# Kernel optimization log

Measured on AMD Instinct MI355X. Metric: run time of the kernel, lower is better.

Reference implementation:

```python
import jax, jax.numpy as jnp
import numpy as np

B, S, D, H = 4, 2048, 1024, 16
HD = D // H  # head dim = 64


def setup_inputs() -> dict:
    key = jax.random.key(0)
    ks = jax.random.split(key, 10)
    std = 1.0 / np.sqrt(D)
    return {
        "Q": jax.random.normal(ks[0], (B, S, D), jnp.float32),
        "Q_lev": jax.random.normal(ks[1], (B, S, D), jnp.float32),
        "K": jax.random.normal(ks[2], (B, S, D), jnp.float32),
        "K_lev": jax.random.normal(ks[3], (B, S, D), jnp.float32),
        "V": jax.random.normal(ks[4], (B, S, D), jnp.float32),
        "V_lev": jax.random.normal(ks[5], (B, S, D), jnp.float32),
        "Wq": jax.random.normal(ks[6], (D, D), jnp.float32) * std,
        "bq": jnp.zeros((D,), jnp.float32),
        "Wk": jax.random.normal(ks[7], (D, D), jnp.float32) * std,
        "bk": jnp.zeros((D,), jnp.float32),
        "Wv": jax.random.normal(ks[8], (D, D), jnp.float32) * std,
        "bv": jnp.zeros((D,), jnp.float32),
        "Wo": jax.random.normal(ks[9], (D, D), jnp.float32) * std,
        "bo": jnp.zeros((D,), jnp.float32),
    }


def _heads(x):
    # [B,S,D] -> [B,H,S,HD]
    return x.reshape(B, S, H, HD).transpose(0, 2, 1, 3)


def reference(Q, Q_lev, K, K_lev, V, V_lev, Wq, bq, Wk, bk, Wv, bv, Wo, bo):
    q = _heads(Q @ Wq + bq + Q_lev)
    k = _heads(K @ Wk + bk + K_lev)
    v = _heads(V @ Wv + bv + V_lev)
    scores = jnp.einsum("bhqd,bhkd->bhqk", q, k) / np.sqrt(HD).astype(np.float32)
    probs = jax.nn.softmax(scores, axis=-1)  # attn_dropout rate 0 -> identity
    ctx = jnp.einsum("bhqk,bhkd->bhqd", probs, v)
    ctx = ctx.transpose(0, 2, 1, 3).reshape(B, S, D)
    return ctx @ Wo + bo  # proj_dropout rate 0 -> identity
```

## Files before the change

### kernel.cpp

```cpp
#include <hip/hip_runtime.h>
#include <hip/hip_bf16.h>

#define Bq 4
#define Sq 2048
#define Dq 1024
#define Hq 16
#define HDq 64
#define MR (Bq*Sq)

typedef __attribute__((ext_vector_type(8))) short bf16x8;
typedef __attribute__((ext_vector_type(4))) float f32x4;
typedef __attribute__((ext_vector_type(16))) float f32x16;

__device__ __forceinline__ unsigned short f2bf(float f){
  unsigned int x = __builtin_bit_cast(unsigned int, f);
  x += 0x7fffu + ((x >> 16) & 1u);
  return (unsigned short)(x >> 16);
}

#define MFMA(a,b,c)   __builtin_amdgcn_mfma_f32_16x16x32_bf16((a),(b),(c),0,0,0)
#define MFMA32(a,b,c) __builtin_amdgcn_mfma_f32_32x32x16_bf16((a),(b),(c),0,0,0)

#define SC_Q 0.18033688f

__global__ __launch_bounds__(256) void transpose_w(
    const float* __restrict__ W0, const float* __restrict__ W1,
    const float* __restrict__ W2, const float* __restrict__ W3,
    unsigned short* __restrict__ T0, unsigned short* __restrict__ T1,
    unsigned short* __restrict__ T2, unsigned short* __restrict__ T3)
{
  __shared__ float tile[32][33];
  const int z = blockIdx.z;
  const float* W = z==0?W0 : z==1?W1 : z==2?W2 : W3;
  unsigned short* T = z==0?T0 : z==1?T1 : z==2?T2 : T3;
  const int k0 = blockIdx.x*32, n0 = blockIdx.y*32;
  const int tx = threadIdx.x & 31, ty = threadIdx.x >> 5;
  #pragma unroll
  for (int i=0;i<4;i++) tile[ty+i*8][tx] = W[(size_t)(k0+ty+i*8)*Dq + n0+tx];
  __syncthreads();
  #pragma unroll
  for (int i=0;i<4;i++) T[(size_t)(n0+ty+i*8)*Dq + k0+tx] = f2bf(tile[tx][ty+i*8]);
}

__global__ __launch_bounds__(256) void transpose_v(
    const unsigned short* __restrict__ Vb, unsigned short* __restrict__ Vo)
{
  __shared__ unsigned short t2[64][72];
  const int bh = blockIdx.y;
  const int b = bh >> 4, h = bh & 15;
  const int s0 = blockIdx.x * 64;
  const int tid = threadIdx.x;
  const int r = tid >> 3, c8 = tid & 7;
  #pragma unroll
  for (int i=0;i<2;i++){
    int s = r + i*32;
    union { int4 v; unsigned short u[8]; } uu;
    uu.v = *(const int4*)(Vb + ((size_t)b*Sq + s0 + s)*Dq + h*HDq + c8*8);
    #pragma unroll
    for (int jj=0;jj<8;jj++){
      int j = (jj + c8) & 7;
      t2[c8*8 + j][s] = uu.u[j];
    }
  }
  __syncthreads();
  #pragma unroll
  for (int i=0;i<2;i++){
    int d = r + i*32;
    *(int4*)(Vo + ((size_t)bh*HDq + d)*Sq + s0 + c8*8) = *(const int4*)&t2[d][c8*8];
  }
}

template<bool AF32>
__device__ __forceinline__ void gemm_loop(const void* __restrict__ Ap,
    const unsigned short* __restrict__ Bt,
    int bm, int bn, unsigned short* Al, unsigned short* Bl, f32x4 acc[4][4])
{
  const int tid = threadIdx.x;
  const int lane = tid & 63, wid = tid >> 6;
  const int lr = lane & 15, lg = lane >> 4;
  const int wm = wid >> 1, wn = wid & 1;

  for (int k0 = 0; k0 < Dq; k0 += 64) {
    __syncthreads();
    if (AF32) {
      const float* A = (const float*)Ap;
      #pragma unroll
      for (int i=0;i<8;i++){
        int slot = tid + 256*i;
        int row = slot >> 4, sl = slot & 15;
        const float4 d = *(const float4*)(A + (size_t)(bm*128+row)*Dq + k0 + sl*4);
        union { unsigned short u[4]; unsigned long long v; } pk;
        pk.u[0]=f2bf(d.x); pk.u[1]=f2bf(d.y); pk.u[2]=f2bf(d.z); pk.u[3]=f2bf(d.w);
        *(unsigned long long*)(Al + row*72 + sl*4) = pk.v;
      }
    } else {
      const unsigned short* A = (const unsigned short*)Ap;
      #pragma unroll
      for (int i=0;i<4;i++){
        int slot = tid + 256*i;
        int row = slot >> 3, sl = slot & 7;
        *(int4*)(Al + row*72 + sl*8) = *(const int4*)(A + (size_t)(bm*128+row)*Dq + k0 + sl*8);
      }
    }
    #pragma unroll
    for (int i=0;i<4;i++){
      int slot = tid + 256*i;
      int row = slot >> 3, sl = slot & 7;
      *(int4*)(Bl + row*72 + sl*8) = *(const int4*)(Bt + (size_t)(bn*128+row)*Dq + k0 + sl*8);
    }
    __syncthreads();
    #pragma unroll
    for (int kc=0;kc<2;kc++){
      bf16x8 af[4], bfr[4];
      #pragma unroll
      for (int mt=0;mt<4;mt++) af[mt]  = *(const bf16x8*)(Al + (wm*64+mt*16+lr)*72 + kc*32 + lg*8);
      #pragma unroll
      for (int nt=0;nt<4;nt++) bfr[nt] = *(const bf16x8*)(Bl + (wn*64+nt*16+lr)*72 + kc*32 + lg*8);
      #pragma unroll
      for (int mt=0;mt<4;mt++)
        #pragma unroll
        for (int nt=0;nt<4;nt++)
          acc[mt][nt] = MFMA(af[mt], bfr[nt], acc[mt][nt]);
    }
  }
}

__global__ __launch_bounds__(256) void proj_gemm(
    const float* __restrict__ Aq, const float* __restrict__ Ak, const float* __restrict__ Av,
    const float* __restrict__ Lq, const float* __restrict__ Lk, const float* __restrict__ Lv,
    const unsigned short* __restrict__ Tq, const unsigned short* __restrict__ Tk, const unsigned short* __restrict__ Tv,
    const float* __restrict__ bqp, const float* __restrict__ bkp, const float* __restrict__ bvp,
    unsigned short* __restrict__ Oq, unsigned short* __restrict__ Ok, unsigned short* __restrict__ Ov)
{
  __shared__ unsigned short Al[128*72];
  __shared__ unsigned short Bl[128*72];
  const int z = blockIdx.z;
  const float* A   = z==0?Aq : z==1?Ak : Av;
  const float* Lev = z==0?Lq : z==1?Lk : Lv;
  const unsigned short* Bt = z==0?Tq : z==1?Tk : Tv;
  const float* bias = z==0?bqp : z==1?bkp : bvp;
  unsigned short* Out = z==0?Oq : z==1?Ok : Ov;
  const float scl = (z==0) ? SC_Q : 1.0f;

  f32x4 acc[4][4];
  #pragma unroll
  for (int mt=0;mt<4;mt++)
    #pragma unroll
    for (int nt=0;nt<4;nt++) acc[mt][nt] = (f32x4){0.f,0.f,0.f,0.f};

  gemm_loop<true>(A, Bt, blockIdx.x, blockIdx.y, Al, Bl, acc);

  const int tid = threadIdx.x, lane = tid&63, wid = tid>>6;
  const int lr = lane&15, lg = lane>>4, wm = wid>>1, wn = wid&1;
  const int colb = blockIdx.y*128 + wn*64;
  float bcol[4];
  #pragma unroll
  for (int nt=0;nt<4;nt++) bcol[nt] = bias[colb + nt*16 + lr];
  #pragma unroll
  for (int mt=0;mt<4;mt++){
    int g = blockIdx.x*128 + wm*64 + mt*16 + lg*4;
    #pragma unroll
    for (int r=0;r<4;r++){
      size_t ro = (size_t)(g+r)*Dq;
      #pragma unroll
      for (int nt=0;nt<4;nt++){
        int col = colb + nt*16 + lr;
        float v = (acc[mt][nt][r] + bcol[nt] + Lev[ro + col]) * scl;
        Out[ro + col] = f2bf(v);
      }
    }
  }
}

__device__ __forceinline__ float comb_max(float x){ return fmaxf(x, __shfl_xor(x, 32, 64)); }
__device__ __forceinline__ float comb_sum(float x){ return x + __shfl_xor(x, 32, 64); }

__device__ __forceinline__ void pack_p(const f32x16& t, int hi, bf16x8& c0, bf16x8& c1){
  unsigned w[8];
  #pragma unroll
  for (int j=0;j<8;j++)
    w[j] = (unsigned)f2bf(t[2*j]) | ((unsigned)f2bf(t[2*j+1]) << 16);
  unsigned x[8];
  #pragma unroll
  for (int j=0;j<8;j++) x[j] = (unsigned)__shfl_xor((int)w[j], 32, 64);
  union { unsigned u[4]; bf16x8 v; } p0, p1;
  p0.u[0] = hi ? x[2] : w[0];
  p0.u[1] = hi ? x[3] : w[1];
  p0.u[2] = hi ? w[2] : x[0];
  p0.u[3] = hi ? w[3] : x[1];
  p1.u[0] = hi ? x[6] : w[4];
  p1.u[1] = hi ? x[7] : w[5];
  p1.u[2] = hi ? w[6] : x[4];
  p1.u[3] = hi ? w[7] : x[5];
  c0 = p0.v; c1 = p1.v;
}

__global__ __launch_bounds__(512, 4) void attn_k(
    const unsigned short* qb, const unsigned short* __restrict__ kb,
    const unsigned short* __restrict__ vt, unsigned short* cb)
{
  __shared__ unsigned short Kl[2][64*64];
  __shared__ unsigned short Vl[2][64*64];
  __shared__ float Rl[8][32];

  const int bid = blockIdx.x;
  const int swz = (bid & 7)*64 + (bid >> 3);
  const int qt = swz & 7, bh = swz >> 3;
  const int b = bh >> 4, h = bh & 15;
  const size_t base = (size_t)b*Sq*Dq + (size_t)h*HDq;

  const int tid = threadIdx.x, lane = tid & 63, wid = tid >> 6;
  const int ln31 = lane & 31, hi = lane >> 5;
  const int q0 = qt*256 + wid*32;

  bf16x8 qf[4];
  {
    const unsigned short* qp = qb + base + (size_t)(q0 + ln31)*Dq + hi*8;
    #pragma unroll
    for (int dk=0;dk<4;dk++) qf[dk] = *(const bf16x8*)(qp + dk*16);
  }

  const int kRow = tid >> 3, kCh = tid & 7;
  const unsigned short* kSrc = kb + base + (size_t)kRow*Dq + kCh*8;
  const unsigned short* vSrc = vt + ((size_t)bh*HDq + kRow)*Sq + kCh*8;
  const int wOff = kRow*64 + ((kCh ^ (kRow & 7))*8);

  int4 kreg = *(const int4*)kSrc;
  int4 vreg = *(const int4*)vSrc;
  *(int4*)&Kl[0][wOff] = kreg;
  *(int4*)&Vl[0][wOff] = vreg;

  f32x16 o0 = (f32x16)(0.0f), o1 = (f32x16)(0.0f);
  float m = -1e30f, l = 0.f;

  for (int kt = 0; kt < Sq/64; ++kt){
    __syncthreads();
    const int p = kt & 1;
    if (kt+1 < Sq/64){
      kreg = *(const int4*)(kSrc + (size_t)(kt+1)*64*Dq);
      vreg = *(const int4*)(vSrc + (kt+1)*64);
    }

    f32x16 t0 = (f32x16)(0.0f), t1 = (f32x16)(0.0f);
    __builtin_amdgcn_s_setprio(1);
    #pragma unroll
    for (int dk=0;dk<4;dk++){
      const int c = hi + dk*2;
      bf16x8 kf0 = *(const bf16x8*)&Kl[p][(ln31)*64    + ((c ^ (ln31 & 7))*8)];
      bf16x8 kf1 = *(const bf16x8*)&Kl[p][(32+ln31)*64 + ((c ^ (ln31 & 7))*8)];
      t0 = MFMA32(kf0, qf[dk], t0);
      t1 = MFMA32(kf1, qf[dk], t1);
    }
    __builtin_amdgcn_s_setprio(0);

    float tmax = t0[0];
    #pragma unroll
    for (int r=1;r<16;r++) tmax = fmaxf(tmax, t0[r]);
    #pragma unroll
    for (int r=0;r<16;r++) tmax = fmaxf(tmax, t1[r]);
    tmax = comb_max(tmax);
    if (__any(tmax > m + 8.0f)){
      float mn = fmaxf(m, tmax);
      float al = __builtin_amdgcn_exp2f(m - mn);
      m = mn;
      l *= al;
      if (hi == 0) Rl[wid][ln31] = al;
      asm volatile("" ::: "memory");
      f32x4 av[4];
      #pragma unroll
      for (int g=0; g<4; g++) av[g] = *(const f32x4*)&Rl[wid][g*8 + hi*4];
      #pragma unroll
      for (int r=0;r<16;r++){ o0[r] *= av[r>>2][r&3]; o1[r] *= av[r>>2][r&3]; }
    }
    float tsum = 0.f;
    #pragma unroll
    for (int r=0;r<16;r++){
      float a0 = __builtin_amdgcn_exp2f(t0[r] - m); t0[r] = a0; tsum += a0;
      float a1 = __builtin_amdgcn_exp2f(t1[r] - m); t1[r] = a1; tsum += a1;
    }
    l += comb_sum(tsum);

    bf16x8 pa0, pa1, pa2, pa3;
    pack_p(t0, hi, pa0, pa1);
    pack_p(t1, hi, pa2, pa3);
    __builtin_amdgcn_s_setprio(1);
    #pragma unroll
    for (int c=0;c<4;c++){
      bf16x8 pa = c==0?pa0 : c==1?pa1 : c==2?pa2 : pa3;
      const int vc = 2*c + hi;
      bf16x8 vf0 = *(const bf16x8*)&Vl[p][(ln31)*64    + ((vc ^ (ln31 & 7))*8)];
      bf16x8 vf1 = *(const bf16x8*)&Vl[p][(32+ln31)*64 + ((vc ^ (ln31 & 7))*8)];
      o0 = MFMA32(pa, vf0, o0);
      o1 = MFMA32(pa, vf1, o1);
    }
    __builtin_amdgcn_s_setprio(0);

    if (kt+1 < Sq/64){
      const int pn = p ^ 1;
      *(int4*)&Kl[pn][wOff] = kreg;
      *(int4*)&Vl[pn][wOff] = vreg;
    }
  }

  float linv = __builtin_amdgcn_rcpf(l);
  if (hi == 0) Rl[wid][ln31] = linv;
  asm volatile("" ::: "memory");
  f32x4 lv[4];
  #pragma unroll
  for (int g=0; g<4; g++) lv[g] = *(const f32x4*)&Rl[wid][g*8 + hi*4];
  #pragma unroll
  for (int r=0;r<16;r++){
    int q = (r&3) + 8*(r>>2) + 4*hi;
    size_t ro = base + (size_t)(q0 + q)*Dq;
    cb[ro + ln31]      = f2bf(o0[r] * lv[r>>2][r&3]);
    cb[ro + 32 + ln31] = f2bf(o1[r] * lv[r>>2][r&3]);
  }
}

__global__ __launch_bounds__(256) void out_gemm(
    const unsigned short* __restrict__ Ctx, const unsigned short* __restrict__ To,
    const float* __restrict__ bop, float* __restrict__ Out)
{
  __shared__ unsigned short Al[128*72];
  __shared__ unsigned short Bl[128*72];
  f32x4 acc[4][4];
  #pragma unroll
  for (int mt=0;mt<4;mt++)
    #pragma unroll
    for (int nt=0;nt<4;nt++) acc[mt][nt] = (f32x4){0.f,0.f,0.f,0.f};

  gemm_loop<false>(Ctx, To, blockIdx.x, blockIdx.y, Al, Bl, acc);

  const int tid = threadIdx.x, lane = tid&63, wid = tid>>6;
  const int lr = lane&15, lg = lane>>4, wm = wid>>1, wn = wid&1;
  const int colb = blockIdx.y*128 + wn*64;
  float bcol[4];
  #pragma unroll
  for (int nt=0;nt<4;nt++) bcol[nt] = bop[colb + nt*16 + lr];
  #pragma unroll
  for (int mt=0;mt<4;mt++){
    int g = blockIdx.x*128 + wm*64 + mt*16 + lg*4;
    #pragma unroll
    for (int r=0;r<4;r++){
      size_t ro = (size_t)(g+r)*Dq;
      #pragma unroll
      for (int nt=0;nt<4;nt++){
        int col = colb + nt*16 + lr;
        Out[ro + col] = acc[mt][nt][r] + bcol[nt];
      }
    }
  }
}

extern "C" void kernel_launch(void* const* d_in, const int* in_sizes, int n_in,
                              void* d_out, int out_size, void* d_ws, size_t ws_size,
                              hipStream_t stream) {
  const float* Q    = (const float*)d_in[0];
  const float* Qlev = (const float*)d_in[1];
  const float* K    = (const float*)d_in[2];
  const float* Klev = (const float*)d_in[3];
  const float* V    = (const float*)d_in[4];
  const float* Vlev = (const float*)d_in[5];
  const float* Wq   = (const float*)d_in[6];
  const float* bq   = (const float*)d_in[7];
  const float* Wk   = (const float*)d_in[8];
  const float* bk   = (const float*)d_in[9];
  const float* Wv   = (const float*)d_in[10];
  const float* bv   = (const float*)d_in[11];
  const float* Wo   = (const float*)d_in[12];
  const float* bo   = (const float*)d_in[13];

  unsigned short* qbuf = (unsigned short*)d_ws;
  unsigned short* kbuf = qbuf + (size_t)MR*Dq;
  unsigned short* vbuf = kbuf + (size_t)MR*Dq;
  unsigned short* vtb  = vbuf + (size_t)MR*Dq;
  unsigned short* Tq   = vtb  + (size_t)MR*Dq;
  unsigned short* Tk   = Tq + (size_t)Dq*Dq;
  unsigned short* Tv   = Tk + (size_t)Dq*Dq;
  unsigned short* To   = Tv + (size_t)Dq*Dq;

  transpose_w<<<dim3(Dq/32, Dq/32, 4), 256, 0, stream>>>(Wq,Wk,Wv,Wo, Tq,Tk,Tv,To);
  proj_gemm<<<dim3(MR/128, Dq/128, 3), 256, 0, stream>>>(
      Q,K,V, Qlev,Klev,Vlev, Tq,Tk,Tv, bq,bk,bv, qbuf,kbuf,vbuf);
  transpose_v<<<dim3(Sq/64, Bq*Hq), 256, 0, stream>>>(vbuf, vtb);
  attn_k<<<dim3(512), 512, 0, stream>>>(qbuf, kbuf, vtb, qbuf);
  out_gemm<<<dim3(MR/128, Dq/128), 256, 0, stream>>>(qbuf, To, bo, (float*)d_out);
}
```

Measured before the change: 273.0 us.

## Pre-convert activations to bf16 and stage GEMM tiles with direct global-to-LDS loads

```diff
diff --git a/kernel.cpp b/kernel.cpp
--- a/kernel.cpp
+++ b/kernel.cpp
@@ -23,6 +23,28 @@
 
 #define SC_Q 0.18033688f
 
+__device__ __forceinline__ void gload16(const unsigned short* g, unsigned short* l){
+  __builtin_amdgcn_global_load_lds(
+      (const __attribute__((address_space(1))) void*)g,
+      (__attribute__((address_space(3))) void*)l, 16, 0, 0);
+}
+
+__global__ __launch_bounds__(256) void cvt_bf16x3(
+    const float* __restrict__ X0, const float* __restrict__ X1, const float* __restrict__ X2,
+    unsigned short* __restrict__ O0, unsigned short* __restrict__ O1, unsigned short* __restrict__ O2)
+{
+  const int z = blockIdx.y;
+  const float* X = z==0?X0 : z==1?X1 : X2;
+  unsigned short* O = z==0?O0 : z==1?O1 : O2;
+  const size_t i = ((size_t)blockIdx.x*256 + threadIdx.x)*8;
+  const float4 a = *(const float4*)(X+i);
+  const float4 b = *(const float4*)(X+i+4);
+  union { unsigned short u[8]; int4 v; } pk;
+  pk.u[0]=f2bf(a.x); pk.u[1]=f2bf(a.y); pk.u[2]=f2bf(a.z); pk.u[3]=f2bf(a.w);
+  pk.u[4]=f2bf(b.x); pk.u[5]=f2bf(b.y); pk.u[6]=f2bf(b.z); pk.u[7]=f2bf(b.w);
+  *(int4*)(O+i) = pk.v;
+}
+
 __global__ __launch_bounds__(256) void transpose_w(
     const float* __restrict__ W0, const float* __restrict__ W1,
     const float* __restrict__ W2, const float* __restrict__ W3,
@@ -70,8 +92,7 @@
   }
 }
 
-template<bool AF32>
-__device__ __forceinline__ void gemm_loop(const void* __restrict__ Ap,
+__device__ __forceinline__ void gemm_loop(const unsigned short* __restrict__ A,
     const unsigned short* __restrict__ Bt,
     int bm, int bn, unsigned short* Al, unsigned short* Bl, f32x4 acc[4][4])
 {
@@ -80,42 +101,28 @@
   const int lr = lane & 15, lg = lane >> 4;
   const int wm = wid >> 1, wn = wid & 1;
 
+  const int srow = wid*32 + (lane >> 3), sch = (lane & 7)*8;
+  const unsigned short* As = A  + (size_t)(bm*128 + srow)*Dq + sch;
+  const unsigned short* Bs = Bt + (size_t)(bn*128 + srow)*Dq + sch;
+  unsigned short* Ald = Al + wid*2048;
+  unsigned short* Bld = Bl + wid*2048;
+
   for (int k0 = 0; k0 < Dq; k0 += 64) {
     __syncthreads();
-    if (AF32) {
-      const float* A = (const float*)Ap;
-      #pragma unroll
-      for (int i=0;i<8;i++){
-        int slot = tid + 256*i;
-        int row = slot >> 4, sl = slot & 15;
-        const float4 d = *(const float4*)(A + (size_t)(bm*128+row)*Dq + k0 + sl*4);
-        union { unsigned short u[4]; unsigned long long v; } pk;
-        pk.u[0]=f2bf(d.x); pk.u[1]=f2bf(d.y); pk.u[2]=f2bf(d.z); pk.u[3]=f2bf(d.w);
-        *(unsigned long long*)(Al + row*72 + sl*4) = pk.v;
-      }
-    } else {
-      const unsigned short* A = (const unsigned short*)Ap;
-      #pragma unroll
-      for (int i=0;i<4;i++){
-        int slot = tid + 256*i;
-        int row = slot >> 3, sl = slot & 7;
-        *(int4*)(Al + row*72 + sl*8) = *(const int4*)(A + (size_t)(bm*128+row)*Dq + k0 + sl*8);
-      }
-    }
     #pragma unroll
     for (int i=0;i<4;i++){
-      int slot = tid + 256*i;
-      int row = slot >> 3, sl = slot & 7;
-      *(int4*)(Bl + row*72 + sl*8) = *(const int4*)(Bt + (size_t)(bn*128+row)*Dq + k0 + sl*8);
-    }
+      gload16(As + (size_t)i*8*Dq + k0, Ald + i*512);
+      gload16(Bs + (size_t)i*8*Dq + k0, Bld + i*512);
+    }
+    asm volatile("s_waitcnt vmcnt(0)" ::: "memory");
     __syncthreads();
     #pragma unroll
     for (int kc=0;kc<2;kc++){
       bf16x8 af[4], bfr[4];
       #pragma unroll
-      for (int mt=0;mt<4;mt++) af[mt]  = *(const bf16x8*)(Al + (wm*64+mt*16+lr)*72 + kc*32 + lg*8);
-      #pragma unroll
-      for (int nt=0;nt<4;nt++) bfr[nt] = *(const bf16x8*)(Bl + (wn*64+nt*16+lr)*72 + kc*32 + lg*8);
+      for (int mt=0;mt<4;mt++) af[mt]  = *(const bf16x8*)(Al + (wm*64+mt*16+lr)*64 + kc*32 + lg*8);
+      #pragma unroll
+      for (int nt=0;nt<4;nt++) bfr[nt] = *(const bf16x8*)(Bl + (wn*64+nt*16+lr)*64 + kc*32 + lg*8);
       #pragma unroll
       for (int mt=0;mt<4;mt++)
         #pragma unroll
@@ -126,16 +133,16 @@
 }
 
 __global__ __launch_bounds__(256) void proj_gemm(
-    const float* __restrict__ Aq, const float* __restrict__ Ak, const float* __restrict__ Av,
+    const unsigned short* __restrict__ Aq, const unsigned short* __restrict__ Ak, const unsigned short* __restrict__ Av,
     const float* __restrict__ Lq, const float* __restrict__ Lk, const float* __restrict__ Lv,
     const unsigned short* __restrict__ Tq, const unsigned short* __restrict__ Tk, const unsigned short* __restrict__ Tv,
     const float* __restrict__ bqp, const float* __restrict__ bkp, const float* __restrict__ bvp,
     unsigned short* __restrict__ Oq, unsigned short* __restrict__ Ok, unsigned short* __restrict__ Ov)
 {
-  __shared__ unsigned short Al[128*72];
-  __shared__ unsigned short Bl[128*72];
+  __shared__ __align__(16) unsigned short Al[128*64];
+  __shared__ __align__(16) unsigned short Bl[128*64];
   const int z = blockIdx.z;
-  const float* A   = z==0?Aq : z==1?Ak : Av;
+  const unsigned short* A = z==0?Aq : z==1?Ak : Av;
   const float* Lev = z==0?Lq : z==1?Lk : Lv;
   const unsigned short* Bt = z==0?Tq : z==1?Tk : Tv;
   const float* bias = z==0?bqp : z==1?bkp : bvp;
@@ -148,7 +155,7 @@
     #pragma unroll
     for (int nt=0;nt<4;nt++) acc[mt][nt] = (f32x4){0.f,0.f,0.f,0.f};
 
-  gemm_loop<true>(A, Bt, blockIdx.x, blockIdx.y, Al, Bl, acc);
+  gemm_loop(A, Bt, blockIdx.x, blockIdx.y, Al, Bl, acc);
 
   const int tid = threadIdx.x, lane = tid&63, wid = tid>>6;
   const int lr = lane&15, lg = lane>>4, wm = wid>>1, wn = wid&1;
@@ -321,15 +328,15 @@
     const unsigned short* __restrict__ Ctx, const unsigned short* __restrict__ To,
     const float* __restrict__ bop, float* __restrict__ Out)
 {
-  __shared__ unsigned short Al[128*72];
-  __shared__ unsigned short Bl[128*72];
+  __shared__ __align__(16) unsigned short Al[128*64];
+  __shared__ __align__(16) unsigned short Bl[128*64];
   f32x4 acc[4][4];
   #pragma unroll
   for (int mt=0;mt<4;mt++)
     #pragma unroll
     for (int nt=0;nt<4;nt++) acc[mt][nt] = (f32x4){0.f,0.f,0.f,0.f};
 
-  gemm_loop<false>(Ctx, To, blockIdx.x, blockIdx.y, Al, Bl, acc);
+  gemm_loop(Ctx, To, blockIdx.x, blockIdx.y, Al, Bl, acc);
 
   const int tid = threadIdx.x, lane = tid&63, wid = tid>>6;
   const int lr = lane&15, lg = lane>>4, wm = wid>>1, wn = wid&1;
@@ -373,15 +380,19 @@
   unsigned short* qbuf = (unsigned short*)d_ws;
   unsigned short* kbuf = qbuf + (size_t)MR*Dq;
   unsigned short* vbuf = kbuf + (size_t)MR*Dq;
-  unsigned short* vtb  = vbuf + (size_t)MR*Dq;
-  unsigned short* Tq   = vtb  + (size_t)MR*Dq;
+  unsigned short* xq   = vbuf + (size_t)MR*Dq;
+  unsigned short* xk   = xq   + (size_t)MR*Dq;
+  unsigned short* xv   = xk   + (size_t)MR*Dq;
+  unsigned short* Tq   = xv   + (size_t)MR*Dq;
   unsigned short* Tk   = Tq + (size_t)Dq*Dq;
   unsigned short* Tv   = Tk + (size_t)Dq*Dq;
   unsigned short* To   = Tv + (size_t)Dq*Dq;
-
+  unsigned short* vtb  = xq;
+
+  cvt_bf16x3<<<dim3(MR*Dq/(256*8), 3), 256, 0, stream>>>(Q, K, V, xq, xk, xv);
   transpose_w<<<dim3(Dq/32, Dq/32, 4), 256, 0, stream>>>(Wq,Wk,Wv,Wo, Tq,Tk,Tv,To);
   proj_gemm<<<dim3(MR/128, Dq/128, 3), 256, 0, stream>>>(
-      Q,K,V, Qlev,Klev,Vlev, Tq,Tk,Tv, bq,bk,bv, qbuf,kbuf,vbuf);
+      xq,xk,xv, Qlev,Klev,Vlev, Tq,Tk,Tv, bq,bk,bv, qbuf,kbuf,vbuf);
   transpose_v<<<dim3(Sq/64, Bq*Hq), 256, 0, stream>>>(vbuf, vtb);
   attn_k<<<dim3(512), 512, 0, stream>>>(qbuf, kbuf, vtb, qbuf);
   out_gemm<<<dim3(MR/128, Dq/128), 256, 0, stream>>>(qbuf, To, bo, (float*)d_out);
```

After: 288.4 us. 1.06x slower.
